# Optimization experiments

Measured on AMD Instinct MI355X. Metric: run time of the kernel, lower is better.

## Reference

```python
import jax, jax.numpy as jnp
import numpy as np

D_MODEL = 1024
N_HEADS = 16
HEAD_DIM = D_MODEL // N_HEADS


def setup_inputs() -> dict:
    key = jax.random.key(0)
    ks = jax.random.split(key, 6)
    B, T, S = 4, 1024, 2048
    scale = 1.0 / np.sqrt(D_MODEL)
    return {
        "query": jax.random.normal(ks[0], (B, T, D_MODEL), jnp.float32),
        "key_value": jax.random.normal(ks[1], (B, S, D_MODEL), jnp.float32),
        "wq": jax.random.normal(ks[2], (D_MODEL, D_MODEL), jnp.float32) * scale,
        "wk": jax.random.normal(ks[3], (D_MODEL, D_MODEL), jnp.float32) * scale,
        "wv": jax.random.normal(ks[4], (D_MODEL, D_MODEL), jnp.float32) * scale,
        "wo": jax.random.normal(ks[5], (D_MODEL, D_MODEL), jnp.float32) * scale,
    }


def reference(query, key_value, wq, wk, wv, wo):
    B, T, _ = query.shape
    S = key_value.shape[1]
    # projections (nn.Linear with weight W computes x @ W.T; here wq etc. are W)
    q = (query @ wq.T).reshape(B, T, N_HEADS, HEAD_DIM)
    k = (key_value @ wk.T).reshape(B, S, N_HEADS, HEAD_DIM)
    v = (key_value @ wv.T).reshape(B, S, N_HEADS, HEAD_DIM)
    scale = HEAD_DIM ** -0.5
    attn = jnp.einsum("bthd,bshd->bhts", q, k) * scale  # [B,H,T,S]
    attn = jax.nn.softmax(attn, axis=-1)
    out = jnp.einsum("bhts,bshd->bthd", attn, v).reshape(B, T, N_HEADS * HEAD_DIM)
    return out @ wo.T
```

## Files before the change

### kernel.cpp

```cpp
#include <hip/hip_runtime.h>
#include <cstdint>
#include <cstddef>

#define N_HEADS 16

typedef __attribute__((ext_vector_type(4))) float f32x4;
typedef __attribute__((ext_vector_type(8))) short bf16x8;

static __device__ inline ushort f2bf(float x) {
    uint32_t u = __float_as_uint(x);
    uint32_t r = (u + 0x7fffu + ((u >> 16) & 1u)) >> 16;
    return (ushort)r;
}
static __device__ inline float bf2f(ushort h) {
    return __uint_as_float(((uint32_t)h) << 16);
}
static __device__ inline uint32_t cvt_pk_bf16(float lo, float hi) {
    uint32_t r;
    asm("v_cvt_pk_bf16_f32 %0, %1, %2" : "=v"(r) : "v"(lo), "v"(hi));
    return r;
}
static __device__ inline float exp2_raw(float x) {
    float r;
    asm("v_exp_f32 %0, %1" : "=v"(r) : "v"(x));
    return r;
}

__global__ __launch_bounds__(256) void split_all(
    const float* __restrict__ query, const float* __restrict__ keyv,
    const float* __restrict__ wq, const float* __restrict__ wk,
    const float* __restrict__ wv, const float* __restrict__ wo,
    ushort* __restrict__ inq_h, ushort* __restrict__ inkv_h,
    ushort* __restrict__ wqh, ushort* __restrict__ wkh,
    ushort* __restrict__ wvh, ushort* __restrict__ woh,
    ushort* __restrict__ wol) {
    const float* x;
    ushort* hi;
    ushort* lo = nullptr;
    int n4;
    switch (blockIdx.y) {
        case 0: x = query; hi = inq_h;           n4 = 1048576; break;
        case 1: x = keyv;  hi = inkv_h;          n4 = 2097152; break;
        case 2: x = wq;    hi = wqh;             n4 = 262144;  break;
        case 3: x = wk;    hi = wkh;             n4 = 262144;  break;
        case 4: x = wv;    hi = wvh;             n4 = 262144;  break;
        default: x = wo;   hi = woh; lo = wol;   n4 = 262144;  break;
    }
    const int stride = gridDim.x * blockDim.x;
    const bool wlo = (lo != nullptr);
    for (int i = blockIdx.x * blockDim.x + threadIdx.x; i < n4; i += stride) {
        const float4 v = reinterpret_cast<const float4*>(x)[i];
        ushort4 h;
        h.x = f2bf(v.x); h.y = f2bf(v.y); h.z = f2bf(v.z); h.w = f2bf(v.w);
        reinterpret_cast<ushort4*>(hi)[i] = h;
        if (wlo) {
            ushort4 l;
            l.x = f2bf(v.x - bf2f(h.x)); l.y = f2bf(v.y - bf2f(h.y));
            l.z = f2bf(v.z - bf2f(h.z)); l.w = f2bf(v.w - bf2f(h.w));
            reinterpret_cast<ushort4*>(lo)[i] = l;
        }
    }
}

#define BM 128
#define BN 128
#define BK 32

#define GLD_LDS16(gp, lp)                                                  \
    __builtin_amdgcn_global_load_lds(                                      \
        (const __attribute__((address_space(1))) void*)(gp),               \
        (__attribute__((address_space(3))) void*)(lp), 16, 0, 0)

__global__ __launch_bounds__(256, 3) void qkv_proj(
    const ushort* __restrict__ Aq, const ushort* __restrict__ Akv,
    const ushort* __restrict__ Wqh, const ushort* __restrict__ Wkh,
    const ushort* __restrict__ Wvh, ushort* __restrict__ aq,
    ushort* __restrict__ ak, ushort* __restrict__ avt) {
    constexpr int K = 1024;
    constexpr int NT = K / BK;
    constexpr float QSCALE = 0.18033688011112042f;
    __shared__ ushort sA[2][BM * BK];
    __shared__ ushort sB[2][BN * BK];

    const int bid = blockIdx.x;
    int seg, local, nrow;
    if (bid < 256)      { seg = 0; local = bid;       nrow = 32; }
    else if (bid < 768) { seg = 1; local = bid - 256; nrow = 64; }
    else                { seg = 2; local = bid - 768; nrow = 64; }
    local = (local & 7) * nrow + (local >> 3);
    const int n0 = (local & 7) * BN;
    const int m0 = (local >> 3) * BM;

    const ushort* A  = (seg == 0) ? Aq : Akv;
    const ushort* Wh = (seg == 0) ? Wqh : (seg == 1 ? Wkh : Wvh);

    const int tid = threadIdx.x;
    const int lane = tid & 63;
    const int w = tid >> 6;
    const int wm = (w >> 1) * 64;
    const int wn = (w & 1) * 64;

    int srow[2], skq[2];
#pragma unroll
    for (int c = 0; c < 2; ++c) {
        const int row = (w * 2 + c) * 16 + (lane >> 2);
        srow[c] = row;
        skq[c] = (((lane & 3) ^ ((row >> 1) & 3)) << 3);
    }

    auto stage = [&](int buf, int k0) {
#pragma unroll
        for (int c = 0; c < 2; ++c) {
            const size_t ga = (size_t)(m0 + srow[c]) * K + k0 + skq[c];
            const size_t gb = (size_t)(n0 + srow[c]) * K + k0 + skq[c];
            const int loff = (w * 2 + c) * 512;
            GLD_LDS16(A + ga, &sA[buf][loff]);
            GLD_LDS16(Wh + gb, &sB[buf][loff]);
        }
    };

    f32x4 acc[4][4];
#pragma unroll
    for (int i = 0; i < 4; ++i)
#pragma unroll
        for (int j = 0; j < 4; ++j) acc[i][j] = (f32x4)0.0f;

    const int lr = lane & 15;
    const int kq = lane >> 4;

    stage(0, 0);
    __syncthreads();

    for (int t = 0; t < NT; ++t) {
        const int bi = t & 1;
        if (t + 1 < NT) stage(bi ^ 1, (t + 1) * BK);

        bf16x8 afh[4], bfh[4];
#pragma unroll
        for (int f = 0; f < 4; ++f) {
            const int arow = wm + f * 16 + lr;
            afh[f] = *reinterpret_cast<const bf16x8*>(
                &sA[bi][arow * 32 + ((kq ^ ((arow >> 1) & 3)) << 3)]);
            const int brow = wn + f * 16 + lr;
            bfh[f] = *reinterpret_cast<const bf16x8*>(
                &sB[bi][brow * 32 + ((kq ^ ((brow >> 1) & 3)) << 3)]);
        }
#pragma unroll
        for (int i = 0; i < 4; ++i)
#pragma unroll
            for (int j = 0; j < 4; ++j)
                acc[i][j] = __builtin_amdgcn_mfma_f32_16x16x32_bf16(
                    afh[i], bfh[j], acc[i][j], 0, 0, 0);
        __syncthreads();
    }

    const int cr = (lane >> 4) << 2;
    const int cc = lane & 15;

    if (seg < 2) {
        const int log2X = (seg == 0) ? 10 : 11;
        const float scale = (seg == 0) ? QSCALE : 1.0f;
        ushort* out = (seg == 0) ? aq : ak;
        const int xm = (1 << log2X) - 1;
#pragma unroll
        for (int i = 0; i < 4; ++i)
#pragma unroll
            for (int j = 0; j < 4; ++j) {
                const int col = n0 + wn + j * 16 + cc;
                const int h = col >> 6, dd = col & 63;
#pragma unroll
                for (int r = 0; r < 4; ++r) {
                    const int mr = m0 + wm + i * 16 + cr + r;
                    const int bb = mr >> log2X;
                    const int x = mr & xm;
                    out[(((size_t)(bb * N_HEADS + h) << log2X) + x) * 64 +
                        (dd ^ ((x & 7) << 3))] = f2bf(acc[i][j][r] * scale);
                }
            }
    } else {
#pragma unroll
        for (int i = 0; i < 4; ++i)
#pragma unroll
            for (int j = 0; j < 4; ++j) {
                const int col = n0 + wn + j * 16 + cc;
                const int h = col >> 6, dd = col & 63;
                const int sb = m0 + wm + i * 16 + cr;
                const int bb = sb >> 11;
                const int sx = sb & 2047;
                ushort4 hv;
#pragma unroll
                for (int r = 0; r < 4; ++r)
                    ((ushort*)&hv)[r] = f2bf(acc[i][j][r]);
                const size_t pos =
                    ((size_t)(bb * N_HEADS + h) * 64 + dd) * 2048 +
                    (sx & ~63) + ((sx & 63) ^ ((dd & 7) << 3));
                *reinterpret_cast<ushort4*>(&avt[pos]) = hv;
            }
    }
}

#define OBM 64
__global__ __launch_bounds__(256, 2) void gemm_oproj(
    const ushort* __restrict__ Ahi, const ushort* __restrict__ Whi,
    const ushort* __restrict__ Wlo, float* __restrict__ Cf, int M, int N,
    int K) {
    __shared__ ushort sA[2][OBM * BK];
    __shared__ ushort sB[2][2][BN * BK];

    const int tid = threadIdx.x;
    const int lane = tid & 63;
    const int w = tid >> 6;
    const int m0 = blockIdx.y * OBM;
    const int n0 = blockIdx.x * BN;
    const int NT = K / BK;

    const int sarow = w * 16 + (lane >> 2);
    const int saq = (((lane & 3) ^ ((sarow >> 1) & 3)) << 3);
    int srow[2], skq[2];
#pragma unroll
    for (int c = 0; c < 2; ++c) {
        const int row = (w * 2 + c) * 16 + (lane >> 2);
        srow[c] = row;
        skq[c] = (((lane & 3) ^ ((row >> 1) & 3)) << 3);
    }

    auto stage = [&](int buf, int k0) {
        GLD_LDS16(Ahi + (size_t)(m0 + sarow) * K + k0 + saq,
                  &sA[buf][w * 512]);
#pragma unroll
        for (int c = 0; c < 2; ++c) {
            const size_t gb = (size_t)(n0 + srow[c]) * K + k0 + skq[c];
            const int loff = (w * 2 + c) * 512;
            GLD_LDS16(Whi + gb, &sB[buf][0][loff]);
            GLD_LDS16(Wlo + gb, &sB[buf][1][loff]);
        }
    };

    f32x4 acc[8];
#pragma unroll
    for (int j = 0; j < 8; ++j) acc[j] = (f32x4)0.0f;

    const int lr = lane & 15;
    const int kq = lane >> 4;

    stage(0, 0);
    __syncthreads();

    for (int t = 0; t < NT; ++t) {
        const int bi = t & 1;
        if (t + 1 < NT) stage(bi ^ 1, (t + 1) * BK);

        const int arow = w * 16 + lr;
        const bf16x8 afh = *reinterpret_cast<const bf16x8*>(
            &sA[bi][arow * 32 + ((kq ^ ((arow >> 1) & 3)) << 3)]);
#pragma unroll
        for (int j = 0; j < 8; ++j) {
            const int brow = j * 16 + lr;
            const int boff = brow * 32 + ((kq ^ ((brow >> 1) & 3)) << 3);
            const bf16x8 bfh =
                *reinterpret_cast<const bf16x8*>(&sB[bi][0][boff]);
            const bf16x8 bfl =
                *reinterpret_cast<const bf16x8*>(&sB[bi][1][boff]);
            acc[j] = __builtin_amdgcn_mfma_f32_16x16x32_bf16(afh, bfh,
                                                             acc[j], 0, 0, 0);
            acc[j] = __builtin_amdgcn_mfma_f32_16x16x32_bf16(afh, bfl,
                                                             acc[j], 0, 0, 0);
        }
        __syncthreads();
    }

    const int cr = (lane >> 4) << 2;
    const int cc = lane & 15;
#pragma unroll
    for (int j = 0; j < 8; ++j) {
        float* cp = &Cf[(size_t)(m0 + w * 16 + cr) * N + n0 + j * 16 + cc];
#pragma unroll
        for (int r = 0; r < 4; ++r) cp[(size_t)r * N] = acc[j][r];
    }
}

__global__ __launch_bounds__(256, 4) void attn_mfma(
    const ushort* __restrict__ Qhi, const ushort* __restrict__ Khi,
    const ushort* __restrict__ Vhi, ushort* __restrict__ Ohi) {
    constexpr int T = 1024, S = 2048, NT = S / 64;
    __shared__ ushort sK[2][4096];
    __shared__ ushort sV[2][4096];
    __shared__ ushort sPb[4096];

    const int tid = threadIdx.x;
    const int lane = tid & 63;
    const int w = tid >> 6;
    const int id = blockIdx.x;
    const int wid = (id & 7) * 128 + (id >> 3);
    const int t0 = (wid & 15) * 64;
    const int bh = wid >> 4;
    const int lr = lane & 15;
    const int g = lane >> 4;
    const int swz = (lr & 7) << 3;

    const size_t qbase = ((size_t)bh * T + t0) * 64;
    const size_t kbase = (size_t)bh * S * 64;
    const size_t vbase = (size_t)bh * 64;

    int loff[2];
    const ushort* kp[2];
    const ushort* vp[2];
#pragma unroll
    for (int i = 0; i < 2; ++i) {
        loff[i] = i * 2048 + w * 512 + lane * 8;
        kp[i] = Khi + kbase + loff[i];
        vp[i] = Vhi + (vbase + (loff[i] >> 6)) * S + (loff[i] & 63);
    }

    int rdoff[4][2], pwoff[4], proff[2];
#pragma unroll
    for (int j = 0; j < 4; ++j) {
#pragma unroll
        for (int kk = 0; kk < 2; ++kk)
            rdoff[j][kk] = (j * 16 + lr) * 64 + ((kk * 32 + g * 8) ^ swz);
        pwoff[j] = lr * 64 + ((j * 16 + g * 4) ^ swz);
    }
#pragma unroll
    for (int kk = 0; kk < 2; ++kk)
        proff[kk] = lr * 64 + ((kk * 32 + g * 8) ^ swz);

#pragma unroll
    for (int i = 0; i < 2; ++i) GLD_LDS16(Qhi + qbase + loff[i], &sK[1][loff[i]]);
#pragma unroll
    for (int i = 0; i < 2; ++i) {
        GLD_LDS16(kp[i], &sK[0][loff[i]]);
        GLD_LDS16(vp[i], &sV[0][loff[i]]);
        kp[i] += 4096;
        vp[i] += 64;
    }
    __syncthreads();

    bf16x8 qf[2];
#pragma unroll
    for (int kk = 0; kk < 2; ++kk)
        qf[kk] = *reinterpret_cast<const bf16x8*>(
            &sK[1][(w * 16 + lr) * 64 + ((kk * 32 + g * 8) ^ swz)]);
    __syncthreads();

    ushort* sP = &sPb[w * 1024];

    f32x4 oacc[4];
#pragma unroll
    for (int jd = 0; jd < 4; ++jd) oacc[jd] = (f32x4)0.0f;
    const f32x4 zero4 = (f32x4)0.0f;
    float lpart = 0.0f;

    for (int t = 0; t < NT; ++t) {
        const int bi = t & 1;
        if (t + 1 < NT) {
#pragma unroll
            for (int i = 0; i < 2; ++i) {
                GLD_LDS16(kp[i], &sK[bi ^ 1][loff[i]]);
                GLD_LDS16(vp[i], &sV[bi ^ 1][loff[i]]);
                kp[i] += 4096;
                vp[i] += 64;
            }
        }

        f32x4 sacc[4];
        __builtin_amdgcn_s_setprio(1);
#pragma unroll
        for (int j = 0; j < 4; ++j) {
            const bf16x8 kh0 = *reinterpret_cast<const bf16x8*>(
                &sK[bi][rdoff[j][0]]);
            const bf16x8 kh1 = *reinterpret_cast<const bf16x8*>(
                &sK[bi][rdoff[j][1]]);
            sacc[j] = __builtin_amdgcn_mfma_f32_16x16x32_bf16(
                kh0, qf[0], zero4, 0, 0, 0);
            sacc[j] = __builtin_amdgcn_mfma_f32_16x16x32_bf16(
                kh1, qf[1], sacc[j], 0, 0, 0);
        }
        __builtin_amdgcn_s_setprio(0);

        uint32_t wpk[4][2];
#pragma unroll
        for (int j = 0; j < 4; ++j) {
            const float p0 = exp2_raw(sacc[j][0]);
            const float p1 = exp2_raw(sacc[j][1]);
            const float p2 = exp2_raw(sacc[j][2]);
            const float p3 = exp2_raw(sacc[j][3]);
            lpart += (p0 + p1) + (p2 + p3);
            wpk[j][0] = cvt_pk_bf16(p0, p1);
            wpk[j][1] = cvt_pk_bf16(p2, p3);
        }

#pragma unroll
        for (int j = 0; j < 4; ++j)
            *reinterpret_cast<uint2*>(&sP[pwoff[j]]) =
                make_uint2(wpk[j][0], wpk[j][1]);
        asm volatile("s_waitcnt lgkmcnt(0)" ::: "memory");
        __builtin_amdgcn_sched_barrier(0);

        bf16x8 pf[2];
#pragma unroll
        for (int kk = 0; kk < 2; ++kk)
            pf[kk] = *reinterpret_cast<const bf16x8*>(&sP[proff[kk]]);
        __builtin_amdgcn_s_setprio(1);
#pragma unroll
        for (int jd = 0; jd < 4; ++jd) {
#pragma unroll
            for (int kk = 0; kk < 2; ++kk) {
                const bf16x8 vh = *reinterpret_cast<const bf16x8*>(
                    &sV[bi][rdoff[jd][kk]]);
                oacc[jd] = __builtin_amdgcn_mfma_f32_16x16x32_bf16(
                    pf[kk], vh, oacc[jd], 0, 0, 0);
            }
        }
        __builtin_amdgcn_s_setprio(0);
        __syncthreads();
    }

    float l = lpart;
    l += __shfl_xor(l, 16);
    l += __shfl_xor(l, 32);

    const int b = bh >> 4, h = bh & 15;
    float linv[4];
#pragma unroll
    for (int r = 0; r < 4; ++r) linv[r] = 1.0f / __shfl(l, g * 4 + r);
#pragma unroll
    for (int r = 0; r < 4; ++r) {
        const int q = t0 + w * 16 + g * 4 + r;
        const size_t rowb = ((size_t)(b * T + q)) * 1024 + h * 64;
#pragma unroll
        for (int jd = 0; jd < 4; ++jd)
            Ohi[rowb + jd * 16 + lr] = f2bf(oacc[jd][r] * linv[r]);
    }
}

extern "C" void kernel_launch(void* const* d_in, const int* in_sizes, int n_in,
                              void* d_out, int out_size, void* d_ws, size_t ws_size,
                              hipStream_t stream) {
    const int B = 4, T = 1024, S = 2048, D = 1024;

    const float* query = (const float*)d_in[0];
    const float* keyv  = (const float*)d_in[1];
    const float* wq    = (const float*)d_in[2];
    const float* wk    = (const float*)d_in[3];
    const float* wv    = (const float*)d_in[4];
    const float* wo    = (const float*)d_in[5];
    float* out = (float*)d_out;

    const size_t nQ = (size_t)B * T * D;
    const size_t nK = (size_t)B * S * D;
    const size_t nW = (size_t)D * D;

    uint8_t* p = (uint8_t*)d_ws;
    ushort* inq_h = (ushort*)p;  p += nQ * 2;
    ushort* inkv_h = (ushort*)p; p += nK * 2;
    ushort* wqh = (ushort*)p;    p += nW * 2;
    ushort* wkh = (ushort*)p;    p += nW * 2;
    ushort* wvh = (ushort*)p;    p += nW * 2;
    ushort* woh = (ushort*)p;    p += nW * 2;
    ushort* wol = (ushort*)p;    p += nW * 2;
    ushort* aq_h = (ushort*)p;   p += nQ * 2;
    ushort* ak_h = (ushort*)p;   p += nK * 2;
    ushort* avt_h = (ushort*)p;  p += nK * 2;
    ushort* ao_h = (ushort*)p;   p += nQ * 2;

    const dim3 blk(256);

    split_all<<<dim3(512, 6), blk, 0, stream>>>(
        query, keyv, wq, wk, wv, wo, inq_h, inkv_h, wqh, wkh, wvh, woh, wol);

    qkv_proj<<<dim3(1280), blk, 0, stream>>>(inq_h, inkv_h, wqh, wkh, wvh,
                                             aq_h, ak_h, avt_h);

    attn_mfma<<<dim3((T / 64) * B * N_HEADS), blk, 0, stream>>>(
        aq_h, ak_h, avt_h, ao_h);

    gemm_oproj<<<dim3(D / BN, (B * T) / OBM), blk, 0, stream>>>(
        ao_h, woh, wol, out, B * T, D, D);
}
```

Before: 158.2 us.

## Enlarge QKV projection tile to 256x128 and drop double buffering

The QKV projection GEMM tile grows from 128x128 to 256x128. Each wave now computes a 64x128 sub-tile with 32 accumulators, so each loaded B fragment is reused across more MFMAs and the grid halves to 640 blocks with a matching XCD swizzle. The LDS double buffer is replaced by a single buffer with a sync after each load, so global-to-LDS loads no longer overlap with compute. Occupancy drops from 3 to 2 blocks per CU, and register pressure rises.

```diff
diff --git a/kernel.cpp b/kernel.cpp
--- a/kernel.cpp
+++ b/kernel.cpp
@@ -71,25 +71,26 @@
         (const __attribute__((address_space(1))) void*)(gp),               \
         (__attribute__((address_space(3))) void*)(lp), 16, 0, 0)
 
-__global__ __launch_bounds__(256, 3) void qkv_proj(
+#define QBM 256
+#define QBN 128
+__global__ __launch_bounds__(256, 2) void qkv_proj(
     const ushort* __restrict__ Aq, const ushort* __restrict__ Akv,
     const ushort* __restrict__ Wqh, const ushort* __restrict__ Wkh,
     const ushort* __restrict__ Wvh, ushort* __restrict__ aq,
     ushort* __restrict__ ak, ushort* __restrict__ avt) {
     constexpr int K = 1024;
-    constexpr int NT = K / BK;
     constexpr float QSCALE = 0.18033688011112042f;
-    __shared__ ushort sA[2][BM * BK];
-    __shared__ ushort sB[2][BN * BK];
+    __shared__ ushort sA[QBM * BK];
+    __shared__ ushort sB[QBN * BK];
 
     const int bid = blockIdx.x;
-    int seg, local, nrow;
-    if (bid < 256)      { seg = 0; local = bid;       nrow = 32; }
-    else if (bid < 768) { seg = 1; local = bid - 256; nrow = 64; }
-    else                { seg = 2; local = bid - 768; nrow = 64; }
-    local = (local & 7) * nrow + (local >> 3);
-    const int n0 = (local & 7) * BN;
-    const int m0 = (local >> 3) * BM;
+    int seg, local, nxcd;
+    if (bid < 128)      { seg = 0; local = bid;       nxcd = 16; }
+    else if (bid < 384) { seg = 1; local = bid - 128; nxcd = 32; }
+    else                { seg = 2; local = bid - 384; nxcd = 32; }
+    local = (local & 7) * nxcd + (local >> 3);
+    const int n0 = (local & 7) * QBN;
+    const int m0 = (local >> 3) * QBM;
 
     const ushort* A  = (seg == 0) ? Aq : Akv;
     const ushort* Wh = (seg == 0) ? Wqh : (seg == 1 ? Wkh : Wvh);
@@ -97,58 +98,60 @@
     const int tid = threadIdx.x;
     const int lane = tid & 63;
     const int w = tid >> 6;
-    const int wm = (w >> 1) * 64;
-    const int wn = (w & 1) * 64;
-
-    int srow[2], skq[2];
+    const int wm = w * 64;
+
+    int sarow[4], sakq[4];
+#pragma unroll
+    for (int c = 0; c < 4; ++c) {
+        const int row = (w * 4 + c) * 16 + (lane >> 2);
+        sarow[c] = row;
+        sakq[c] = (((lane & 3) ^ ((row >> 1) & 3)) << 3);
+    }
+    int sbrow[2], sbkq[2];
 #pragma unroll
     for (int c = 0; c < 2; ++c) {
         const int row = (w * 2 + c) * 16 + (lane >> 2);
-        srow[c] = row;
-        skq[c] = (((lane & 3) ^ ((row >> 1) & 3)) << 3);
-    }
-
-    auto stage = [&](int buf, int k0) {
-#pragma unroll
-        for (int c = 0; c < 2; ++c) {
-            const size_t ga = (size_t)(m0 + srow[c]) * K + k0 + skq[c];
-            const size_t gb = (size_t)(n0 + srow[c]) * K + k0 + skq[c];
-            const int loff = (w * 2 + c) * 512;
-            GLD_LDS16(A + ga, &sA[buf][loff]);
-            GLD_LDS16(Wh + gb, &sB[buf][loff]);
-        }
-    };
-
-    f32x4 acc[4][4];
+        sbrow[c] = row;
+        sbkq[c] = (((lane & 3) ^ ((row >> 1) & 3)) << 3);
+    }
+
+    f32x4 acc[4][8];
 #pragma unroll
     for (int i = 0; i < 4; ++i)
 #pragma unroll
-        for (int j = 0; j < 4; ++j) acc[i][j] = (f32x4)0.0f;
+        for (int j = 0; j < 8; ++j) acc[i][j] = (f32x4)0.0f;
 
     const int lr = lane & 15;
     const int kq = lane >> 4;
 
-    stage(0, 0);
-    __syncthreads();
-
-    for (int t = 0; t < NT; ++t) {
-        const int bi = t & 1;
-        if (t + 1 < NT) stage(bi ^ 1, (t + 1) * BK);
-
-        bf16x8 afh[4], bfh[4];
+    for (int k0 = 0; k0 < K; k0 += BK) {
+#pragma unroll
+        for (int c = 0; c < 4; ++c)
+            GLD_LDS16(A + (size_t)(m0 + sarow[c]) * K + k0 + sakq[c],
+                      &sA[(w * 4 + c) * 512]);
+#pragma unroll
+        for (int c = 0; c < 2; ++c)
+            GLD_LDS16(Wh + (size_t)(n0 + sbrow[c]) * K + k0 + sbkq[c],
+                      &sB[(w * 2 + c) * 512]);
+        __syncthreads();
+
+        bf16x8 afh[4], bfh[8];
 #pragma unroll
         for (int f = 0; f < 4; ++f) {
             const int arow = wm + f * 16 + lr;
             afh[f] = *reinterpret_cast<const bf16x8*>(
-                &sA[bi][arow * 32 + ((kq ^ ((arow >> 1) & 3)) << 3)]);
-            const int brow = wn + f * 16 + lr;
-            bfh[f] = *reinterpret_cast<const bf16x8*>(
-                &sB[bi][brow * 32 + ((kq ^ ((brow >> 1) & 3)) << 3)]);
+                &sA[arow * 32 + ((kq ^ ((arow >> 1) & 3)) << 3)]);
+        }
+#pragma unroll
+        for (int j = 0; j < 8; ++j) {
+            const int brow = j * 16 + lr;
+            bfh[j] = *reinterpret_cast<const bf16x8*>(
+                &sB[brow * 32 + ((kq ^ ((brow >> 1) & 3)) << 3)]);
         }
 #pragma unroll
         for (int i = 0; i < 4; ++i)
 #pragma unroll
-            for (int j = 0; j < 4; ++j)
+            for (int j = 0; j < 8; ++j)
                 acc[i][j] = __builtin_amdgcn_mfma_f32_16x16x32_bf16(
                     afh[i], bfh[j], acc[i][j], 0, 0, 0);
         __syncthreads();
@@ -165,8 +168,8 @@
 #pragma unroll
         for (int i = 0; i < 4; ++i)
 #pragma unroll
-            for (int j = 0; j < 4; ++j) {
-                const int col = n0 + wn + j * 16 + cc;
+            for (int j = 0; j < 8; ++j) {
+                const int col = n0 + j * 16 + cc;
                 const int h = col >> 6, dd = col & 63;
 #pragma unroll
                 for (int r = 0; r < 4; ++r) {
@@ -181,8 +184,8 @@
 #pragma unroll
         for (int i = 0; i < 4; ++i)
 #pragma unroll
-            for (int j = 0; j < 4; ++j) {
-                const int col = n0 + wn + j * 16 + cc;
+            for (int j = 0; j < 8; ++j) {
+                const int col = n0 + j * 16 + cc;
                 const int h = col >> 6, dd = col & 63;
                 const int sb = m0 + wm + i * 16 + cr;
                 const int bb = sb >> 11;
@@ -468,8 +471,8 @@
     split_all<<<dim3(512, 6), blk, 0, stream>>>(
         query, keyv, wq, wk, wv, wo, inq_h, inkv_h, wqh, wkh, wvh, woh, wol);
 
-    qkv_proj<<<dim3(1280), blk, 0, stream>>>(inq_h, inkv_h, wqh, wkh, wvh,
-                                             aq_h, ak_h, avt_h);
+    qkv_proj<<<dim3(640), blk, 0, stream>>>(inq_h, inkv_h, wqh, wkh, wvh,
+                                            aq_h, ak_h, avt_h);
 
     attn_mfma<<<dim3((T / 64) * B * N_HEADS), blk, 0, stream>>>(
         aq_h, ak_h, avt_h, ao_h);
```

Result: slower. 164.5 us (+4.0%).
